# Kernel optimization log

Measured on AMD Instinct MI355X. Metric: run time of the kernel, lower is better.

The kernel has to match this reference:

```python
import jax, jax.numpy as jnp
import numpy as np

EPS = 1e-5

def _layernorm(x, w, b):
    mu = jnp.mean(x, axis=-1, keepdims=True)
    var = jnp.var(x, axis=-1, keepdims=True)
    return (x - mu) * jax.lax.rsqrt(var + EPS) * w + b

def setup_inputs() -> dict:
    key = jax.random.key(0)
    ks = jax.random.split(key, 7)
    b, n, m, d, h = 4, 1024, 1024, 1024, 16
    sc = 1.0 / np.sqrt(d)
    return {
        "x": jax.random.normal(ks[0], (b, n, d), jnp.float32),
        "xa": jax.random.normal(ks[1], (b, m, d), jnp.float32),
        "ln_w": jnp.ones((d,), jnp.float32),
        "ln_b": jnp.zeros((d,), jnp.float32),
        "Wq": jax.random.normal(ks[2], (d, d), jnp.float32) * sc,
        "Wkv": jax.random.normal(ks[3], (d, 2 * d), jnp.float32) * sc,
        "Wout": jax.random.normal(ks[4], (d, d), jnp.float32) * sc,
    }

def reference(x, xa, ln_w, ln_b, Wq, Wkv, Wout):
    b, n, d = x.shape
    m = xa.shape[1]
    h = 16
    hd = d // h

    xn = _layernorm(x, ln_w, ln_b)
    xan = _layernorm(xa, ln_w, ln_b)

    q = xn @ Wq                      # [b,n,d]
    kv = xn @ Wkv                    # [b,n,2d] (k,v unused for x->xa path except v)
    k, v = kv[..., :d], kv[..., d:]
    kva = xan @ Wkv
    ka, va = kva[..., :d], kva[..., d:]

    split = lambda t: t.reshape(t.shape[0], t.shape[1], h, hd).transpose(0, 2, 1, 3)  # [b,h,s,hd]
    q, v, ka, va = map(split, (q, v, ka, va))

    # shared score matrix: scores[b,h,n,m] = q . ka  (no scaling in source)
    scores = jnp.einsum('bhnd,bhmd->bhnm', q, ka)
    # x -> attends over xa: softmax over m
    probs_x = jax.nn.softmax(scores, axis=-1)
    x_upd = jnp.einsum('bhnm,bhmd->bhnd', probs_x, va)
    # xa -> attends over x: softmax over n (of transposed scores)
    probs_xa = jax.nn.softmax(scores.transpose(0, 1, 3, 2), axis=-1)  # [b,h,m,n]
    xa_upd = jnp.einsum('bhmn,bhnd->bhmd', probs_xa, v)

    merge = lambda t: t.transpose(0, 2, 1, 3).reshape(t.shape[0], t.shape[2], d)
    return (merge(x_upd) @ Wout, merge(xa_upd) @ Wout)
```

## Files before the change

kernel.cpp:

```cpp
#include <hip/hip_runtime.h>
#include <hip/hip_bf16.h>

typedef unsigned short u16;
typedef unsigned int u32;
typedef __attribute__((ext_vector_type(4))) unsigned short u16x4;
typedef __attribute__((ext_vector_type(8))) unsigned short u16x8;
typedef __attribute__((ext_vector_type(8))) __bf16 bf16x8;
typedef __attribute__((ext_vector_type(4))) float f32x4;

__device__ __forceinline__ u16 f2bf(float f){
  unsigned u = __builtin_bit_cast(unsigned, f);
  u += 0x7FFFu + ((u >> 16) & 1u);
  return (u16)(u >> 16);
}

__device__ __forceinline__ u32 cvtpk(float lo, float hi){
  u32 r;
  asm("v_cvt_pk_bf16_f32 %0, %1, %2" : "=v"(r) : "v"(lo), "v"(hi));
  return r;
}

__device__ __forceinline__ void load_lds16(const void* g, void* l){
  __builtin_amdgcn_global_load_lds((const __attribute__((address_space(1))) unsigned*)g,
                                   (__attribute__((address_space(3))) unsigned*)l, 16, 0, 0);
}

__device__ __forceinline__ void storeC(float* p, float v){ *p = v; }
__device__ __forceinline__ void storeC(u16* p, float v){ *p = f2bf(v); }

__global__ __launch_bounds__(256) void prep(const float* __restrict__ x, const float* __restrict__ xa,
                                            const float* __restrict__ w, const float* __restrict__ bb,
                                            const float* __restrict__ Wq, const float* __restrict__ Wkv,
                                            const float* __restrict__ Wout,
                                            u16* __restrict__ xn, u16* __restrict__ xan,
                                            u16* __restrict__ WqT, u16* __restrict__ WkT,
                                            u16* __restrict__ WvT, u16* __restrict__ WoT){
  __shared__ float tile[64][65];
  int bid = blockIdx.x, t = threadIdx.x;
  if (bid < 8192){
    int row = bid;
    const float* src; u16* dst;
    if (row < 4096){ src = x + (size_t)row * 1024; dst = xn + (size_t)row * 1024; }
    else { src = xa + (size_t)(row - 4096) * 1024; dst = xan + (size_t)(row - 4096) * 1024; }
    float4 v = ((const float4*)src)[t];
    float s = v.x + v.y + v.z + v.w;
    float ss = v.x*v.x + v.y*v.y + v.z*v.z + v.w*v.w;
#pragma unroll
    for (int o = 32; o > 0; o >>= 1){ s += __shfl_down(s, o); ss += __shfl_down(ss, o); }
    float* red = &tile[0][0];
    int wv = t >> 6;
    if ((t & 63) == 0){ red[wv] = s; red[wv + 4] = ss; }
    __syncthreads();
    if (t == 0){
      red[0] = red[0] + red[1] + red[2] + red[3];
      red[4] = red[4] + red[5] + red[6] + red[7];
    }
    __syncthreads();
    float mu = red[0] * (1.0f/1024.0f);
    float var = red[4] * (1.0f/1024.0f) - mu*mu;
    float rstd = rsqrtf(var + 1e-5f);
    float4 wv4 = ((const float4*)w)[t];
    float4 bv4 = ((const float4*)bb)[t];
    u16x4 o4;
    o4.x = f2bf((v.x - mu) * rstd * wv4.x + bv4.x);
    o4.y = f2bf((v.y - mu) * rstd * wv4.y + bv4.y);
    o4.z = f2bf((v.z - mu) * rstd * wv4.z + bv4.z);
    o4.w = f2bf((v.w - mu) * rstd * wv4.w + bv4.w);
    ((u16x4*)dst)[t] = o4;
    return;
  }
  int tt = bid - 8192;
  int z = tt >> 8, rem = tt & 255;
  int bx = rem & 15, by = rem >> 4;
  const float* in; u16* out; int ldin;
  switch (z){
    case 0:  in = Wq;         out = WqT; ldin = 1024; break;
    case 1:  in = Wkv;        out = WkT; ldin = 2048; break;
    case 2:  in = Wkv + 1024; out = WvT; ldin = 2048; break;
    default: in = Wout;       out = WoT; ldin = 1024; break;
  }
  float scl = (z == 0) ? 1.44269504f : 1.0f;
  int tr = by * 64, tc = bx * 64;
  int r0 = t >> 4, c0 = (t & 15) * 4;
#pragma unroll
  for (int i = 0; i < 4; ++i){
    int r = r0 + i * 16;
    const float4 val = *(const float4*)&in[(size_t)(tr + r) * ldin + tc + c0];
    tile[r][c0] = val.x; tile[r][c0+1] = val.y; tile[r][c0+2] = val.z; tile[r][c0+3] = val.w;
  }
  __syncthreads();
#pragma unroll
  for (int i = 0; i < 4; ++i){
    int n = r0 + i * 16;
    u16x4 o4;
    o4.x = f2bf(tile[c0+0][n] * scl); o4.y = f2bf(tile[c0+1][n] * scl);
    o4.z = f2bf(tile[c0+2][n] * scl); o4.w = f2bf(tile[c0+3][n] * scl);
    *(u16x4*)&out[(size_t)(tc + n) * 1024 + tr + c0] = o4;
  }
}

template<int BM, int NQ, int TMASK, typename OutT>
__global__ __launch_bounds__(512, 2) void gemm256(
    const u16* __restrict__ A0, const u16* __restrict__ A1,
    const u16* __restrict__ A2, const u16* __restrict__ A3,
    const u16* __restrict__ B0, const u16* __restrict__ B1,
    const u16* __restrict__ B2, const u16* __restrict__ B3,
    OutT* __restrict__ C0, OutT* __restrict__ C1,
    OutT* __restrict__ C2, OutT* __restrict__ C3){
  constexpr int AI = BM / 64;
  constexpr int FI = BM / 32;
  constexpr int MT = (NQ == 4) ? 16 : 64;
  __shared__ u16 SA[2][BM * 64];
  __shared__ u16 SB[2][16384];
  int tid = threadIdx.x, lane = tid & 63, wave = tid >> 6;
  int g = lane >> 4, r15 = lane & 15;
  int id = blockIdx.x;
  int r8 = id & 7, k = id >> 3;
  int gm = (k >> 2) * 8 + r8;
  int ntile = k & 3;
  int quad = gm / MT;
  int mbase = (gm % MT) * BM, nbase = ntile * 256;
  const u16* A = quad==0?A0:quad==1?A1:quad==2?A2:A3;
  const u16* B = quad==0?B0:quad==1?B1:quad==2?B2:B3;
  OutT* C      = quad==0?C0:quad==1?C1:quad==2?C2:C3;
  int wr = wave >> 2, wc = wave & 3;
  int rsub = lane >> 3;
  int slo  = (lane & 7) ^ ((lane >> 3) & 7);
  int sw8  = (r15 & 7) << 3;
  f32x4 acc[FI][4] = {};

#define STG(kt, b) { \
  int ko = (kt) * 64; \
  _Pragma("unroll") \
  for (int i = 0; i < AI; ++i){ \
    int row = i*64 + wave*8 + rsub; \
    load_lds16(A + (size_t)(mbase + row)*1024 + ko + slo*8, &SA[b][(i*512 + wave*64)*8]); \
  } \
  _Pragma("unroll") \
  for (int i = 0; i < 4; ++i){ \
    int row = i*64 + wave*8 + rsub; \
    load_lds16(B + (size_t)(nbase + row)*1024 + ko + slo*8, &SB[b][(i*512 + wave*64)*8]); \
  } }

  STG(0, 0);
  for (int t = 0; t < 16; ++t){
    int b = t & 1;
    if (t < 15){
      STG(t + 1, b ^ 1);
      if constexpr (AI == 4) asm volatile("s_waitcnt vmcnt(8)" ::: "memory");
      else                   asm volatile("s_waitcnt vmcnt(6)" ::: "memory");
    } else {
      asm volatile("s_waitcnt vmcnt(0)" ::: "memory");
    }
    __builtin_amdgcn_s_barrier();
    __builtin_amdgcn_sched_barrier(0);
    const u16* Al = &SA[b][0];
    const u16* Bl = &SB[b][0];
#pragma unroll
    for (int ks = 0; ks < 2; ++ks){
      bf16x8 af[FI], bfr[4];
#pragma unroll
      for (int fi = 0; fi < FI; ++fi)
        af[fi] = *(const bf16x8*)&Al[(wr*(FI*16) + fi*16 + r15)*64 + ((ks*32 + g*8) ^ sw8)];
#pragma unroll
      for (int fj = 0; fj < 4; ++fj)
        bfr[fj] = *(const bf16x8*)&Bl[(wc*64 + fj*16 + r15)*64 + ((ks*32 + g*8) ^ sw8)];
#pragma unroll
      for (int fi = 0; fi < FI; ++fi)
#pragma unroll
        for (int fj = 0; fj < 4; ++fj)
          acc[fi][fj] = __builtin_amdgcn_mfma_f32_16x16x32_bf16(af[fi], bfr[fj], acc[fi][fj], 0, 0, 0);
    }
    __builtin_amdgcn_s_barrier();
  }
#undef STG

  bool tr = (TMASK >> quad) & 1;
#pragma unroll
  for (int fi = 0; fi < FI; ++fi)
#pragma unroll
    for (int fj = 0; fj < 4; ++fj){
      int colb = nbase + wc*64 + fj*16 + r15;
      int row0 = mbase + wr*(FI*16) + fi*16 + g*4;
      if constexpr (TMASK != 0){
        if (tr){
          int bb = row0 >> 10, token = row0 & 1023;
          int hh = colb >> 6, dd = colb & 63;
          u16x4 o;
          o.x = f2bf(acc[fi][fj][0]); o.y = f2bf(acc[fi][fj][1]);
          o.z = f2bf(acc[fi][fj][2]); o.w = f2bf(acc[fi][fj][3]);
          *(u16x4*)((u16*)C + ((size_t)((bb << 4) + hh) * 64 + dd) * 1024 + token) = o;
          continue;
        }
      }
#pragma unroll
      for (int r = 0; r < 4; ++r)
        storeC(&C[(size_t)(row0 + r) * 1024 + colb], acc[fi][fj][r]);
    }
}

#define SW(row, col) ((row) * 64 + ((col) ^ (((row) & 7) << 3)))

__device__ __forceinline__ void exchP(const f32x4& s0, const f32x4& s1,
                                      const f32x4& s2, const f32x4& s3,
                                      bool gh, bool g0, bf16x8& pf0, bf16x8& pf1){
  u32 pk00 = cvtpk(s0[0], s0[1]), pk01 = cvtpk(s0[2], s0[3]);
  u32 pk10 = cvtpk(s1[0], s1[1]), pk11 = cvtpk(s1[2], s1[3]);
  u32 pk20 = cvtpk(s2[0], s2[1]), pk21 = cvtpk(s2[2], s2[3]);
  u32 pk30 = cvtpk(s3[0], s3[1]), pk31 = cvtpk(s3[2], s3[3]);
  u32 c0 = gh ? pk10 : pk00, c1 = gh ? pk11 : pk01;
  u32 d0 = gh ? pk00 : pk10, d1 = gh ? pk01 : pk11;
  u32 s1a = __shfl_xor((int)c0, 16), s1b = __shfl_xor((int)c1, 16);
  u32 s2a = __shfl_xor((int)d0, 32), s2b = __shfl_xor((int)d1, 32);
  u32 s3a = __shfl_xor((int)d0, 48), s3b = __shfl_xor((int)d1, 48);
  union UB { u32 w[4]; bf16x8 v; } ub0, ub1;
  ub0.w[0] = gh ? (g0 ? s1a : s2a) : (g0 ? s3a : c0);
  ub0.w[1] = gh ? (g0 ? s1b : s2b) : (g0 ? s3b : c1);
  ub0.w[2] = gh ? (g0 ? c0 : s3a) : (g0 ? s2a : s1a);
  ub0.w[3] = gh ? (g0 ? c1 : s3b) : (g0 ? s2b : s1b);
  u32 e0 = gh ? pk30 : pk20, e1 = gh ? pk31 : pk21;
  u32 f0 = gh ? pk20 : pk30, f1 = gh ? pk21 : pk31;
  u32 t1a = __shfl_xor((int)e0, 16), t1b = __shfl_xor((int)e1, 16);
  u32 t2a = __shfl_xor((int)f0, 32), t2b = __shfl_xor((int)f1, 32);
  u32 t3a = __shfl_xor((int)f0, 48), t3b = __shfl_xor((int)f1, 48);
  ub1.w[0] = gh ? (g0 ? t1a : t2a) : (g0 ? t3a : e0);
  ub1.w[1] = gh ? (g0 ? t1b : t2b) : (g0 ? t3b : e1);
  ub1.w[2] = gh ? (g0 ? e0 : t3a) : (g0 ? t2a : t1a);
  ub1.w[3] = gh ? (g0 ? e1 : t3b) : (g0 ? t2b : t1b);
  pf0 = ub0.v; pf1 = ub1.v;
}

#define MFMA16(a, b, c) __builtin_amdgcn_mfma_f32_16x16x32_bf16(a, b, c, 0, 0, 0)

__global__ __launch_bounds__(256) void flash(const u16* __restrict__ qg, const u16* __restrict__ vTg,
                                             const u16* __restrict__ kag, const u16* __restrict__ vaTg,
                                             u16* __restrict__ xu, u16* __restrict__ xau){
  __shared__ u16 Ks[4096], VTs[4096];
  int tid = threadIdx.x, lane = tid & 63, wave = tid >> 6, g = lane >> 4, r15 = lane & 15;
  int b = blockIdx.x;
  int xcd = b & 7, idx = b >> 3;
  int qt = idx & 15;
  int pair = xcd * 16 + (idx >> 4);
  int bh = pair & 63, dir = pair >> 6;
  size_t tokbase = ((size_t)(bh >> 4)) * 1048576 + (size_t)(bh & 15) * 64;
  size_t vtbase  = (size_t)bh << 16;
  const u16 *Q, *K, *VT; u16* O;
  if (dir == 0){ Q = qg + tokbase;  K = kag + tokbase; VT = vaTg + vtbase; O = xu  + tokbase; }
  else         { Q = kag + tokbase; K = qg  + tokbase; VT = vTg  + vtbase; O = xau + tokbase; }
  Q += (size_t)qt * 64 * 1024;
  O += (size_t)qt * 64 * 1024;

  int wq = wave * 16;
  bf16x8 qf0 = *(const bf16x8*)&Q[(size_t)(wq + r15) * 1024 + g*8];
  bf16x8 qf1 = *(const bf16x8*)&Q[(size_t)(wq + r15) * 1024 + 32 + g*8];

  int srow = tid >> 3, scol = (tid & 7) * 8;
  const u16* Kp  = K  + (size_t)srow * 1024 + scol;
  const u16* VTp = VT + (size_t)srow * 1024 + scol;
  u16x8 kr0 = *(const u16x8*)(Kp);
  u16x8 kr1 = *(const u16x8*)(Kp + (size_t)32 * 1024);
  u16x8 vr0 = *(const u16x8*)(VTp);
  u16x8 vr1 = *(const u16x8*)(VTp + (size_t)32 * 1024);

  float l = 0.0f;
  f32x4 acc[4] = {};
  bool gh = g >= 2, g0 = g & 1;
  const f32x4 zinit = {-32.f, -32.f, -32.f, -32.f};

  for (int j = 0; j < 16; ++j){
    __syncthreads();
    *(u16x8*)&Ks [SW(srow,      scol)] = kr0;
    *(u16x8*)&Ks [SW(srow + 32, scol)] = kr1;
    *(u16x8*)&VTs[SW(srow,      scol)] = vr0;
    *(u16x8*)&VTs[SW(srow + 32, scol)] = vr1;
    if (j < 15){
      const u16* Kn = Kp  + (size_t)(j + 1) * 64 * 1024;
      const u16* Vn = VTp + (j + 1) * 64;
      kr0 = *(const u16x8*)(Kn);
      kr1 = *(const u16x8*)(Kn + (size_t)32 * 1024);
      vr0 = *(const u16x8*)(Vn);
      vr1 = *(const u16x8*)(Vn + (size_t)32 * 1024);
    }
    __syncthreads();

    f32x4 sf[4];
    __builtin_amdgcn_s_setprio(1);
#pragma unroll
    for (int kvi = 0; kvi < 4; ++kvi){
      bf16x8 kf0 = *(const bf16x8*)&Ks[SW(kvi*16 + r15, g*8)];
      bf16x8 kf1 = *(const bf16x8*)&Ks[SW(kvi*16 + r15, 32 + g*8)];
      f32x4 z = MFMA16(kf0, qf0, zinit);
      z = MFMA16(kf1, qf1, z);
      sf[kvi] = z;
    }
    __builtin_amdgcn_s_setprio(0);

    float psum = 0.0f;
#pragma unroll
    for (int kvi = 0; kvi < 4; ++kvi)
#pragma unroll
      for (int r = 0; r < 4; ++r){
        float p = __builtin_amdgcn_exp2f(sf[kvi][r]);
        sf[kvi][r] = p; psum += p;
      }
    psum += __shfl_xor(psum, 16);
    psum += __shfl_xor(psum, 32);
    l += psum;

    bf16x8 pf0, pf1;
    exchP(sf[0], sf[1], sf[2], sf[3], gh, g0, pf0, pf1);

    __builtin_amdgcn_s_setprio(1);
#pragma unroll
    for (int nb = 0; nb < 4; ++nb){
      bf16x8 vf0 = *(const bf16x8*)&VTs[SW(nb*16 + r15, g*8)];
      acc[nb] = MFMA16(vf0, pf0, acc[nb]);
    }
#pragma unroll
    for (int nb = 0; nb < 4; ++nb){
      bf16x8 vf1 = *(const bf16x8*)&VTs[SW(nb*16 + r15, 32 + g*8)];
      acc[nb] = MFMA16(vf1, pf1, acc[nb]);
    }
    __builtin_amdgcn_s_setprio(0);
  }

  float inv = 1.0f / l;
  size_t orow = (size_t)(wq + r15) * 1024;
#pragma unroll
  for (int nb = 0; nb < 4; ++nb){
    u16x4 o;
    o.x = f2bf(acc[nb][0] * inv);
    o.y = f2bf(acc[nb][1] * inv);
    o.z = f2bf(acc[nb][2] * inv);
    o.w = f2bf(acc[nb][3] * inv);
    *(u16x4*)&O[orow + nb*16 + g*4] = o;
  }
}

extern "C" void kernel_launch(void* const* d_in, const int* in_sizes, int n_in,
                              void* d_out, int out_size, void* d_ws, size_t ws_size,
                              hipStream_t stream){
  const float* x    = (const float*)d_in[0];
  const float* xa   = (const float*)d_in[1];
  const float* lnw  = (const float*)d_in[2];
  const float* lnb  = (const float*)d_in[3];
  const float* Wq   = (const float*)d_in[4];
  const float* Wkv  = (const float*)d_in[5];
  const float* Wout = (const float*)d_in[6];
  float* out = (float*)d_out;
  char* ws = (char*)d_ws;
  const size_t MB = 1ull << 20;
  u16* xn  = (u16*)(ws);
  u16* xan = (u16*)(ws + 8*MB);
  u16* q   = (u16*)(ws + 16*MB);
  u16* vT  = (u16*)(ws + 24*MB);
  u16* ka  = (u16*)(ws + 32*MB);
  u16* vaT = (u16*)(ws + 40*MB);
  u16* xu  = (u16*)(ws + 48*MB);
  u16* xau = (u16*)(ws + 56*MB);
  u16* WqT = (u16*)(ws + 64*MB);
  u16* WkT = (u16*)(ws + 66*MB);
  u16* WvT = (u16*)(ws + 68*MB);
  u16* WoT = (u16*)(ws + 70*MB);
  dim3 blk(256);
  prep<<<dim3(9216), blk, 0, stream>>>(x, xa, lnw, lnb, Wq, Wkv, Wout,
                                       xn, xan, WqT, WkT, WvT, WoT);
  gemm256<256, 4, 0xA, u16><<<dim3(256), dim3(512), 0, stream>>>(
      xn, xn, xan, xan, WqT, WvT, WkT, WvT, q, vT, ka, vaT);
  flash<<<dim3(2048), blk, 0, stream>>>(q, vT, ka, vaT, xu, xau);
  gemm256<128, 1, 0, float><<<dim3(256), dim3(512), 0, stream>>>(
      xu, xu, xu, xu, WoT, WoT, WoT, WoT, out, out, out, out);
}
```

Measured before the change: 145.5 us.

## Stage K/V tiles via direct global-to-LDS loads and defer row-sum reduction

```diff
diff --git a/kernel.cpp b/kernel.cpp
--- a/kernel.cpp
+++ b/kernel.cpp
@@ -254,34 +254,28 @@
   bf16x8 qf0 = *(const bf16x8*)&Q[(size_t)(wq + r15) * 1024 + g*8];
   bf16x8 qf1 = *(const bf16x8*)&Q[(size_t)(wq + r15) * 1024 + 32 + g*8];
 
-  int srow = tid >> 3, scol = (tid & 7) * 8;
-  const u16* Kp  = K  + (size_t)srow * 1024 + scol;
-  const u16* VTp = VT + (size_t)srow * 1024 + scol;
-  u16x8 kr0 = *(const u16x8*)(Kp);
-  u16x8 kr1 = *(const u16x8*)(Kp + (size_t)32 * 1024);
-  u16x8 vr0 = *(const u16x8*)(VTp);
-  u16x8 vr1 = *(const u16x8*)(VTp + (size_t)32 * 1024);
-
-  float l = 0.0f;
+  int rl = lane >> 3;
+  int ch = (lane & 7) ^ rl;
+  const u16* Kb = K  + (size_t)(wave*8 + rl) * 1024 + ch*8;
+  const u16* Vb = VT + (size_t)(wave*8 + rl) * 1024 + ch*8;
+
+#define FSTG(j) { \
+  load_lds16(Kb + (size_t)(j)*65536,                 &Ks [(wave*8)*64]); \
+  load_lds16(Kb + (size_t)(j)*65536 + 32*1024,       &Ks [(wave*8 + 32)*64]); \
+  load_lds16(Vb + (j)*64,                            &VTs[(wave*8)*64]); \
+  load_lds16(Vb + (j)*64 + (size_t)32*1024,          &VTs[(wave*8 + 32)*64]); \
+}
+
+  float pl = 0.0f;
   f32x4 acc[4] = {};
   bool gh = g >= 2, g0 = g & 1;
   const f32x4 zinit = {-32.f, -32.f, -32.f, -32.f};
 
   for (int j = 0; j < 16; ++j){
-    __syncthreads();
-    *(u16x8*)&Ks [SW(srow,      scol)] = kr0;
-    *(u16x8*)&Ks [SW(srow + 32, scol)] = kr1;
-    *(u16x8*)&VTs[SW(srow,      scol)] = vr0;
-    *(u16x8*)&VTs[SW(srow + 32, scol)] = vr1;
-    if (j < 15){
-      const u16* Kn = Kp  + (size_t)(j + 1) * 64 * 1024;
-      const u16* Vn = VTp + (j + 1) * 64;
-      kr0 = *(const u16x8*)(Kn);
-      kr1 = *(const u16x8*)(Kn + (size_t)32 * 1024);
-      vr0 = *(const u16x8*)(Vn);
-      vr1 = *(const u16x8*)(Vn + (size_t)32 * 1024);
-    }
-    __syncthreads();
+    FSTG(j);
+    asm volatile("s_waitcnt vmcnt(0)" ::: "memory");
+    __builtin_amdgcn_s_barrier();
+    __builtin_amdgcn_sched_barrier(0);
 
     f32x4 sf[4];
     __builtin_amdgcn_s_setprio(1);
@@ -295,17 +289,13 @@
     }
     __builtin_amdgcn_s_setprio(0);
 
-    float psum = 0.0f;
 #pragma unroll
     for (int kvi = 0; kvi < 4; ++kvi)
 #pragma unroll
       for (int r = 0; r < 4; ++r){
         float p = __builtin_amdgcn_exp2f(sf[kvi][r]);
-        sf[kvi][r] = p; psum += p;
+        sf[kvi][r] = p; pl += p;
       }
-    psum += __shfl_xor(psum, 16);
-    psum += __shfl_xor(psum, 32);
-    l += psum;
 
     bf16x8 pf0, pf1;
     exchP(sf[0], sf[1], sf[2], sf[3], gh, g0, pf0, pf1);
@@ -322,9 +312,13 @@
       acc[nb] = MFMA16(vf1, pf1, acc[nb]);
     }
     __builtin_amdgcn_s_setprio(0);
-  }
-
-  float inv = 1.0f / l;
+    __builtin_amdgcn_s_barrier();
+  }
+#undef FSTG
+
+  pl += __shfl_xor(pl, 16);
+  pl += __shfl_xor(pl, 32);
+  float inv = 1.0f / pl;
   size_t orow = (size_t)(wq + r15) * 1024;
 #pragma unroll
   for (int nb = 0; nb < 4; ++nb){
```

Result: faster. 141.1 us, median of 2 (-3.0%).
